# Performance work log

Hardware: AMD Instinct MI355X
Metric: run time of the kernel (lower is better)

The kernel has to match this reference:

```python
import jax, jax.numpy as jnp
import numpy as np
import math

N = 12288
D = 64
SCALE0 = math.log(10.0)


def lorentz_linear(x, W, b, scale):
    # x: [N, D] -> nn.Linear then Lorentz re-normalization onto the hyperboloid
    h = x @ W.T + b
    time = jax.nn.sigmoid(h[:, :1]) * jnp.exp(scale) + 1.1  # [N, 1]
    xn = h[:, 1:]  # spatial components [N, D-1]
    sq = jnp.clip(jnp.sum(xn * xn, axis=-1, keepdims=True), 1e-8, None)
    s = (time * time - 1.0) / sq
    return jnp.concatenate([time, xn * jnp.sqrt(s)], axis=-1)


def setup_inputs() -> dict:
    key = jax.random.key(0)
    ks = jax.random.split(key, 8)
    stdv = 1.0 / math.sqrt(D)
    x = jax.random.normal(ks[0], (N, D), dtype=jnp.float32)
    # sparse-ish binary adjacency stored dense (module calls adj.to_dense())
    adj = (jax.random.uniform(ks[1], (N, N)) < 0.002).astype(jnp.float32)
    W = jax.random.uniform(ks[2], (D, D), minval=-stdv, maxval=stdv, dtype=jnp.float32)
    Wq = jax.random.uniform(ks[3], (D, D), minval=-stdv, maxval=stdv, dtype=jnp.float32)
    Wk = jax.random.uniform(ks[4], (D, D), minval=-stdv, maxval=stdv, dtype=jnp.float32)
    z = jnp.zeros((D,), dtype=jnp.float32)
    sc = jnp.asarray(SCALE0, dtype=jnp.float32)
    return {
        'x': x, 'adj': adj,
        'W': W, 'b': z, 'scale': sc,
        'Wq': Wq, 'bq': z, 'scale_q': sc,
        'Wk': Wk, 'bk': z, 'scale_k': sc,
        'att_bias': jnp.asarray(20.0, dtype=jnp.float32),
        'att_scale': jnp.asarray(math.sqrt(D), dtype=jnp.float32),
    }


def reference(x, adj, W, b, scale, Wq, bq, scale_q, Wk, bk, scale_k, att_bias, att_scale):
    # LorentzLinear
    h = lorentz_linear(x, W, b, scale)  # [N, D]
    # LorentzAgg with attention
    q = lorentz_linear(h, Wq, bq, scale_q)
    k = lorentz_linear(h, Wk, bk, scale_k)
    # cinner: Lorentzian inner product matrix (negate time component of q)
    qm = jnp.concatenate([-q[:, :1], q[:, 1:]], axis=-1)
    att = 2.0 + 2.0 * (qm @ k.T)                 # [N, N]
    att = jax.nn.sigmoid(att / att_scale + att_bias)
    att = adj * att                               # mask by adjacency
    support = att @ h                             # [N, D]
    # Lorentz self-inner: inner(v,v) = -v0^2 + sum(v_rest^2); denorm = sqrt(|-inner|)
    inner = -support[:, :1] ** 2 + jnp.sum(support[:, 1:] ** 2, axis=-1, keepdims=True)
    denorm = jnp.sqrt(jnp.clip(jnp.abs(-inner), 1e-8, None))
    return support / denorm
```

## Files before the change

### kernel.cpp

```cpp
#include <hip/hip_runtime.h>
#include <math.h>

#define N 12288
#define D 64
#define CAP 96

__device__ __forceinline__ float wave_sum(float v) {
    #pragma unroll
    for (int m = 32; m >= 1; m >>= 1) v += __shfl_xor(v, m, 64);
    return v;
}

__global__ void lorentz_linear_kernel(const float* __restrict__ in,
                                      const float* __restrict__ W,
                                      const float* __restrict__ b,
                                      const float* __restrict__ scale,
                                      float* __restrict__ out,
                                      int negFirst) {
    __shared__ float Wlds[D * (D + 1)];
    int tid = threadIdx.x;
    for (int idx = tid; idx < D * D; idx += 256) {
        int d = idx >> 6, kk = idx & 63;
        Wlds[d * (D + 1) + kk] = W[idx];
    }
    __syncthreads();

    int lane = tid & 63;
    int row  = blockIdx.x * 4 + (tid >> 6);

    float xv  = in[row * D + lane];
    float acc = b[lane];
    const float* wr = &Wlds[lane * (D + 1)];
    #pragma unroll
    for (int kk = 0; kk < D; ++kk) {
        float xk = __shfl(xv, kk, 64);
        acc = fmaf(xk, wr[kk], acc);
    }

    float h0   = __shfl(acc, 0, 64);
    float es   = __expf(scale[0]);
    float time = es / (1.0f + __expf(-h0)) + 1.1f;
    float sq   = wave_sum((lane == 0) ? 0.0f : acc * acc);
    sq = fmaxf(sq, 1e-8f);
    float s = (time * time - 1.0f) / sq;
    float r = sqrtf(s);
    float o = (lane == 0) ? (negFirst ? -time : time) : acc * r;
    out[row * D + lane] = o;
}

__global__ void adj_scan_kernel(const float4* __restrict__ adj4,
                                int* __restrict__ cnt,
                                int* __restrict__ cols) {
    const int total = (N / 4) * N;
    int stride = gridDim.x * blockDim.x;
    for (int t = blockIdx.x * blockDim.x + threadIdx.x; t < total; t += stride) {
        float4 v = adj4[t];
        if (v.x == 0.0f && v.y == 0.0f && v.z == 0.0f && v.w == 0.0f) continue;
        int i = t / (N / 4);
        int jbase = (t - i * (N / 4)) * 4;
        float vals[4] = {v.x, v.y, v.z, v.w};
        #pragma unroll
        for (int c = 0; c < 4; ++c) {
            if (vals[c] != 0.0f) {
                int pos = atomicAdd(&cnt[i], 1);
                if (pos < CAP) cols[i * CAP + pos] = jbase + c;
            }
        }
    }
}

__global__ void gather_kernel(const float* __restrict__ qm,
                              const float* __restrict__ kmat,
                              const float* __restrict__ h,
                              const int* __restrict__ cnt,
                              const int* __restrict__ cols,
                              const float* __restrict__ att_bias_p,
                              const float* __restrict__ att_scale_p,
                              float* __restrict__ out) {
    int lane = threadIdx.x & 63;
    int row  = blockIdx.x * 4 + (threadIdx.x >> 6);

    float qv = qm[row * D + lane];
    int m = cnt[row]; if (m > CAP) m = CAP;
    float bias      = att_bias_p[0];
    float inv_scale = 1.0f / att_scale_p[0];

    float acc = 0.0f;
    for (int n = 0; n < m; ++n) {
        int j = cols[row * CAP + n];
        float dot = wave_sum(qv * kmat[j * D + lane]);
        float a   = fmaf(2.0f + 2.0f * dot, inv_scale, bias);
        float att = 1.0f / (1.0f + __expf(-a));
        acc = fmaf(att, h[j * D + lane], acc);
    }

    float contrib = (lane == 0) ? -acc * acc : acc * acc;
    float inner   = wave_sum(contrib);
    float denorm  = sqrtf(fmaxf(fabsf(inner), 1e-8f));
    out[row * D + lane] = acc / denorm;
}

extern "C" void kernel_launch(void* const* d_in, const int* in_sizes, int n_in,
                              void* d_out, int out_size, void* d_ws, size_t ws_size,
                              hipStream_t stream) {
    const float* x         = (const float*)d_in[0];
    const float* adj       = (const float*)d_in[1];
    const float* W         = (const float*)d_in[2];
    const float* b         = (const float*)d_in[3];
    const float* scale     = (const float*)d_in[4];
    const float* Wq        = (const float*)d_in[5];
    const float* bq        = (const float*)d_in[6];
    const float* scale_q   = (const float*)d_in[7];
    const float* Wk        = (const float*)d_in[8];
    const float* bk        = (const float*)d_in[9];
    const float* scale_k   = (const float*)d_in[10];
    const float* att_bias  = (const float*)d_in[11];
    const float* att_scale = (const float*)d_in[12];
    float* out = (float*)d_out;

    float* h    = (float*)d_ws;
    float* qm   = h  + (size_t)N * D;
    float* kmat = qm + (size_t)N * D;
    int*   cnt  = (int*)(kmat + (size_t)N * D);
    int*   cols = cnt + N;

    hipMemsetAsync(cnt, 0, N * sizeof(int), stream);

    lorentz_linear_kernel<<<N / 4, 256, 0, stream>>>(x, W, b, scale, h, 0);
    lorentz_linear_kernel<<<N / 4, 256, 0, stream>>>(h, Wq, bq, scale_q, qm, 1);
    lorentz_linear_kernel<<<N / 4, 256, 0, stream>>>(h, Wk, bk, scale_k, kmat, 0);

    adj_scan_kernel<<<2048, 256, 0, stream>>>((const float4*)adj, cnt, cols);

    gather_kernel<<<N / 4, 256, 0, stream>>>(qm, kmat, h, cnt, cols,
                                             att_bias, att_scale, out);
}
```

Before: 891.5 us.

## Fuse adjacency scan into gather kernel and merge Q/K projections

Each block now scans one adjacency row directly, collecting the nonzero columns in shared memory with LDS atomics. It then splits the neighbor loop across four waves and reduces their partial sums through LDS. This removes the global cnt/cols buffers, the memset, the global atomics and one kernel launch. The Q and K Lorentz projections are also fused into one kernel that reads h once. Using a uint4 bitwise test for zero treats -0.0 as nonzero, which is harmless for a 0/1 adjacency matrix.

```diff
diff --git a/kernel.cpp b/kernel.cpp
--- a/kernel.cpp
+++ b/kernel.cpp
@@ -11,12 +11,16 @@
     return v;
 }
 
-__global__ void lorentz_linear_kernel(const float* __restrict__ in,
-                                      const float* __restrict__ W,
-                                      const float* __restrict__ b,
-                                      const float* __restrict__ scale,
-                                      float* __restrict__ out,
-                                      int negFirst) {
+__device__ __forceinline__ float sigmoidf(float a) {
+    return 1.0f / (1.0f + __expf(-a));
+}
+
+__global__ __launch_bounds__(256) void lorentz_linear_kernel(
+        const float* __restrict__ in,
+        const float* __restrict__ W,
+        const float* __restrict__ b,
+        const float* __restrict__ scale,
+        float* __restrict__ out) {
     __shared__ float Wlds[D * (D + 1)];
     int tid = threadIdx.x;
     for (int idx = tid; idx < D * D; idx += 256) {
@@ -38,66 +42,118 @@
     }
 
     float h0   = __shfl(acc, 0, 64);
-    float es   = __expf(scale[0]);
-    float time = es / (1.0f + __expf(-h0)) + 1.1f;
-    float sq   = wave_sum((lane == 0) ? 0.0f : acc * acc);
-    sq = fmaxf(sq, 1e-8f);
-    float s = (time * time - 1.0f) / sq;
-    float r = sqrtf(s);
-    float o = (lane == 0) ? (negFirst ? -time : time) : acc * r;
-    out[row * D + lane] = o;
+    float time = __expf(scale[0]) * sigmoidf(h0) + 1.1f;
+    float sq   = fmaxf(wave_sum((lane == 0) ? 0.0f : acc * acc), 1e-8f);
+    float r    = sqrtf((time * time - 1.0f) / sq);
+    out[row * D + lane] = (lane == 0) ? time : acc * r;
 }
 
-__global__ void adj_scan_kernel(const float4* __restrict__ adj4,
-                                int* __restrict__ cnt,
-                                int* __restrict__ cols) {
-    const int total = (N / 4) * N;
-    int stride = gridDim.x * blockDim.x;
-    for (int t = blockIdx.x * blockDim.x + threadIdx.x; t < total; t += stride) {
-        float4 v = adj4[t];
-        if (v.x == 0.0f && v.y == 0.0f && v.z == 0.0f && v.w == 0.0f) continue;
-        int i = t / (N / 4);
-        int jbase = (t - i * (N / 4)) * 4;
-        float vals[4] = {v.x, v.y, v.z, v.w};
-        #pragma unroll
-        for (int c = 0; c < 4; ++c) {
-            if (vals[c] != 0.0f) {
-                int pos = atomicAdd(&cnt[i], 1);
-                if (pos < CAP) cols[i * CAP + pos] = jbase + c;
+__global__ __launch_bounds__(256) void lorentz_qk_kernel(
+        const float* __restrict__ h,
+        const float* __restrict__ Wq, const float* __restrict__ bq, const float* __restrict__ scale_q,
+        const float* __restrict__ Wk, const float* __restrict__ bk, const float* __restrict__ scale_k,
+        float* __restrict__ qm, float* __restrict__ kmat) {
+    __shared__ float Wqlds[D * (D + 1)];
+    __shared__ float Wklds[D * (D + 1)];
+    int tid = threadIdx.x;
+    for (int idx = tid; idx < D * D; idx += 256) {
+        int d = idx >> 6, kk = idx & 63;
+        Wqlds[d * (D + 1) + kk] = Wq[idx];
+        Wklds[d * (D + 1) + kk] = Wk[idx];
+    }
+    __syncthreads();
+
+    int lane = tid & 63;
+    int row  = blockIdx.x * 4 + (tid >> 6);
+
+    float hv   = h[row * D + lane];
+    float accq = bq[lane];
+    float acck = bk[lane];
+    const float* wq = &Wqlds[lane * (D + 1)];
+    const float* wk = &Wklds[lane * (D + 1)];
+    #pragma unroll
+    for (int kk = 0; kk < D; ++kk) {
+        float xk = __shfl(hv, kk, 64);
+        accq = fmaf(xk, wq[kk], accq);
+        acck = fmaf(xk, wk[kk], acck);
+    }
+
+    {
+        float h0   = __shfl(accq, 0, 64);
+        float time = __expf(scale_q[0]) * sigmoidf(h0) + 1.1f;
+        float sq   = fmaxf(wave_sum((lane == 0) ? 0.0f : accq * accq), 1e-8f);
+        float r    = sqrtf((time * time - 1.0f) / sq);
+        qm[row * D + lane] = (lane == 0) ? -time : accq * r;
+    }
+    {
+        float h0   = __shfl(acck, 0, 64);
+        float time = __expf(scale_k[0]) * sigmoidf(h0) + 1.1f;
+        float sq   = fmaxf(wave_sum((lane == 0) ? 0.0f : acck * acck), 1e-8f);
+        float r    = sqrtf((time * time - 1.0f) / sq);
+        kmat[row * D + lane] = (lane == 0) ? time : acck * r;
+    }
+}
+
+__global__ __launch_bounds__(256) void adj_gather_kernel(
+        const uint4* __restrict__ adj4,
+        const float* __restrict__ qm,
+        const float* __restrict__ kmat,
+        const float* __restrict__ h,
+        const float* __restrict__ att_bias_p,
+        const float* __restrict__ att_scale_p,
+        float* __restrict__ out) {
+    __shared__ int scols[CAP];
+    __shared__ int scnt;
+    __shared__ float sacc[4][D];
+
+    int tid  = threadIdx.x;
+    int row  = blockIdx.x;
+    if (tid == 0) scnt = 0;
+    __syncthreads();
+
+    const uint4* rowp = adj4 + (size_t)row * (N / 4);
+    #pragma unroll
+    for (int it = 0; it < (N / 4) / 256; ++it) {
+        int t = it * 256 + tid;
+        uint4 v = rowp[t];
+        if ((v.x | v.y | v.z | v.w) != 0u) {
+            unsigned e[4] = {v.x, v.y, v.z, v.w};
+            #pragma unroll
+            for (int c = 0; c < 4; ++c) {
+                if (e[c] != 0u) {
+                    int pos = atomicAdd(&scnt, 1);
+                    if (pos < CAP) scols[pos] = t * 4 + c;
+                }
             }
         }
     }
-}
+    __syncthreads();
 
-__global__ void gather_kernel(const float* __restrict__ qm,
-                              const float* __restrict__ kmat,
-                              const float* __restrict__ h,
-                              const int* __restrict__ cnt,
-                              const int* __restrict__ cols,
-                              const float* __restrict__ att_bias_p,
-                              const float* __restrict__ att_scale_p,
-                              float* __restrict__ out) {
-    int lane = threadIdx.x & 63;
-    int row  = blockIdx.x * 4 + (threadIdx.x >> 6);
+    int m = scnt; if (m > CAP) m = CAP;
+    int lane = tid & 63;
+    int w    = tid >> 6;
 
-    float qv = qm[row * D + lane];
-    int m = cnt[row]; if (m > CAP) m = CAP;
+    float qv        = qm[row * D + lane];
     float bias      = att_bias_p[0];
     float inv_scale = 1.0f / att_scale_p[0];
 
     float acc = 0.0f;
-    for (int n = 0; n < m; ++n) {
-        int j = cols[row * CAP + n];
+    for (int n = w; n < m; n += 4) {
+        int j = scols[n];
         float dot = wave_sum(qv * kmat[j * D + lane]);
-        float a   = fmaf(2.0f + 2.0f * dot, inv_scale, bias);
-        float att = 1.0f / (1.0f + __expf(-a));
+        float att = sigmoidf(fmaf(2.0f + 2.0f * dot, inv_scale, bias));
         acc = fmaf(att, h[j * D + lane], acc);
     }
+    sacc[w][lane] = acc;
+    __syncthreads();
 
-    float contrib = (lane == 0) ? -acc * acc : acc * acc;
-    float inner   = wave_sum(contrib);
-    float denorm  = sqrtf(fmaxf(fabsf(inner), 1e-8f));
-    out[row * D + lane] = acc / denorm;
+    if (w == 0) {
+        float total = sacc[0][lane] + sacc[1][lane] + sacc[2][lane] + sacc[3][lane];
+        float contrib = (lane == 0) ? -total * total : total * total;
+        float inner   = wave_sum(contrib);
+        float denorm  = sqrtf(fmaxf(fabsf(inner), 1e-8f));
+        out[row * D + lane] = total / denorm;
+    }
 }
 
 extern "C" void kernel_launch(void* const* d_in, const int* in_sizes, int n_in,
@@ -121,17 +177,10 @@
     float* h    = (float*)d_ws;
     float* qm   = h  + (size_t)N * D;
     float* kmat = qm + (size_t)N * D;
-    int*   cnt  = (int*)(kmat + (size_t)N * D);
-    int*   cols = cnt + N;
 
-    hipMemsetAsync(cnt, 0, N * sizeof(int), stream);
-
-    lorentz_linear_kernel<<<N / 4, 256, 0, stream>>>(x, W, b, scale, h, 0);
-    lorentz_linear_kernel<<<N / 4, 256, 0, stream>>>(h, Wq, bq, scale_q, qm, 1);
-    lorentz_linear_kernel<<<N / 4, 256, 0, stream>>>(h, Wk, bk, scale_k, kmat, 0);
-
-    adj_scan_kernel<<<2048, 256, 0, stream>>>((const float4*)adj, cnt, cols);
-
-    gather_kernel<<<N / 4, 256, 0, stream>>>(qm, kmat, h, cnt, cols,
+    lorentz_linear_kernel<<<N / 4, 256, 0, stream>>>(x, W, b, scale, h);
+    lorentz_qk_kernel<<<N / 4, 256, 0, stream>>>(h, Wq, bq, scale_q,
+                                                 Wk, bk, scale_k, qm, kmat);
+    adj_gather_kernel<<<N, 256, 0, stream>>>((const uint4*)adj, qm, kmat, h,
                                              att_bias, att_scale, out);
 }
```

Measured after the change: 824.2 us. -7.6%, faster.

## Fuse Lorentz linears and per-row adjacency scan into one kernel

Applied to the files above, without the earlier changes.

Merges the three Lorentz linear kernels and the adjacency scan into a single phase-one kernel. Each wavefront computes h, q and k for its row and then scans that row of adj with nontemporal loads, collecting column indices through LDS atomics before writing them out. This removes the memset, three kernel launches, the global atomics and the intermediate round trip of h between kernels. The cost is that the adjacency streaming, which dominates runtime, now runs inside a kernel with high LDS use, which may lower occupancy.

```diff
diff --git a/kernel.cpp b/kernel.cpp
--- a/kernel.cpp
+++ b/kernel.cpp
@@ -1,87 +1,127 @@
 #include <hip/hip_runtime.h>
 #include <math.h>
 
-#define N 12288
-#define D 64
+#define N   12288
+#define D   64
 #define CAP 96
+
+typedef unsigned int uint4n __attribute__((ext_vector_type(4)));
 
 __device__ __forceinline__ float wave_sum(float v) {
     #pragma unroll
     for (int m = 32; m >= 1; m >>= 1) v += __shfl_xor(v, m, 64);
     return v;
 }
+__device__ __forceinline__ float sigmoidf(float a) { return 1.0f / (1.0f + __expf(-a)); }
 
-__global__ void lorentz_linear_kernel(const float* __restrict__ in,
-                                      const float* __restrict__ W,
-                                      const float* __restrict__ b,
-                                      const float* __restrict__ scale,
-                                      float* __restrict__ out,
-                                      int negFirst) {
-    __shared__ float Wlds[D * (D + 1)];
-    int tid = threadIdx.x;
+__global__ __launch_bounds__(256) void phase1_kernel(
+        const float* __restrict__ x,
+        const uint4n* __restrict__ adj4,
+        const float* __restrict__ W,  const float* __restrict__ b,  const float* __restrict__ scale,
+        const float* __restrict__ Wq, const float* __restrict__ bq, const float* __restrict__ scale_q,
+        const float* __restrict__ Wk, const float* __restrict__ bk, const float* __restrict__ scale_k,
+        float* __restrict__ h, float* __restrict__ qm, float* __restrict__ kmat,
+        int* __restrict__ cnt, int* __restrict__ cols) {
+    __shared__ float Wl [D * (D + 1)];
+    __shared__ float Wql[D * (D + 1)];
+    __shared__ float Wkl[D * (D + 1)];
+    __shared__ unsigned short scols[4][CAP];
+    __shared__ int scnt[4];
+
+    const int tid  = threadIdx.x;
+    const int lane = tid & 63;
+    const int w    = tid >> 6;
+    const int row  = blockIdx.x * 4 + w;
+
     for (int idx = tid; idx < D * D; idx += 256) {
         int d = idx >> 6, kk = idx & 63;
-        Wlds[d * (D + 1) + kk] = W[idx];
+        Wl [d * (D + 1) + kk] = W [idx];
+        Wql[d * (D + 1) + kk] = Wq[idx];
+        Wkl[d * (D + 1) + kk] = Wk[idx];
     }
+    if (lane == 0) scnt[w] = 0;
     __syncthreads();
 
-    int lane = tid & 63;
-    int row  = blockIdx.x * 4 + (tid >> 6);
-
-    float xv  = in[row * D + lane];
-    float acc = b[lane];
-    const float* wr = &Wlds[lane * (D + 1)];
-    #pragma unroll
-    for (int kk = 0; kk < D; ++kk) {
-        float xk = __shfl(xv, kk, 64);
-        acc = fmaf(xk, wr[kk], acc);
+    float hvv;
+    {
+        float xv  = x[row * D + lane];
+        float acc = b[lane];
+        const float* wr = &Wl[lane * (D + 1)];
+        #pragma unroll
+        for (int kk = 0; kk < D; ++kk)
+            acc = fmaf(__shfl(xv, kk, 64), wr[kk], acc);
+        float h0   = __shfl(acc, 0, 64);
+        float time = __expf(scale[0]) * sigmoidf(h0) + 1.1f;
+        float sq   = fmaxf(wave_sum((lane == 0) ? 0.0f : acc * acc), 1e-8f);
+        float r    = sqrtf((time * time - 1.0f) / sq);
+        hvv = (lane == 0) ? time : acc * r;
+        h[row * D + lane] = hvv;
     }
 
-    float h0   = __shfl(acc, 0, 64);
-    float es   = __expf(scale[0]);
-    float time = es / (1.0f + __expf(-h0)) + 1.1f;
-    float sq   = wave_sum((lane == 0) ? 0.0f : acc * acc);
-    sq = fmaxf(sq, 1e-8f);
-    float s = (time * time - 1.0f) / sq;
-    float r = sqrtf(s);
-    float o = (lane == 0) ? (negFirst ? -time : time) : acc * r;
-    out[row * D + lane] = o;
-}
+    {
+        float accq = bq[lane], acck = bk[lane];
+        const float* wq = &Wql[lane * (D + 1)];
+        const float* wk = &Wkl[lane * (D + 1)];
+        #pragma unroll
+        for (int kk = 0; kk < D; ++kk) {
+            float xk = __shfl(hvv, kk, 64);
+            accq = fmaf(xk, wq[kk], accq);
+            acck = fmaf(xk, wk[kk], acck);
+        }
+        {
+            float h0   = __shfl(accq, 0, 64);
+            float time = __expf(scale_q[0]) * sigmoidf(h0) + 1.1f;
+            float sq   = fmaxf(wave_sum((lane == 0) ? 0.0f : accq * accq), 1e-8f);
+            float r    = sqrtf((time * time - 1.0f) / sq);
+            qm[row * D + lane] = (lane == 0) ? -time : accq * r;
+        }
+        {
+            float h0   = __shfl(acck, 0, 64);
+            float time = __expf(scale_k[0]) * sigmoidf(h0) + 1.1f;
+            float sq   = fmaxf(wave_sum((lane == 0) ? 0.0f : acck * acck), 1e-8f);
+            float r    = sqrtf((time * time - 1.0f) / sq);
+            kmat[row * D + lane] = (lane == 0) ? time : acck * r;
+        }
+    }
 
-__global__ void adj_scan_kernel(const float4* __restrict__ adj4,
-                                int* __restrict__ cnt,
-                                int* __restrict__ cols) {
-    const int total = (N / 4) * N;
-    int stride = gridDim.x * blockDim.x;
-    for (int t = blockIdx.x * blockDim.x + threadIdx.x; t < total; t += stride) {
-        float4 v = adj4[t];
-        if (v.x == 0.0f && v.y == 0.0f && v.z == 0.0f && v.w == 0.0f) continue;
-        int i = t / (N / 4);
-        int jbase = (t - i * (N / 4)) * 4;
-        float vals[4] = {v.x, v.y, v.z, v.w};
-        #pragma unroll
-        for (int c = 0; c < 4; ++c) {
-            if (vals[c] != 0.0f) {
-                int pos = atomicAdd(&cnt[i], 1);
-                if (pos < CAP) cols[i * CAP + pos] = jbase + c;
+    {
+        const uint4n* rp = adj4 + (size_t)row * (N / 4);
+        #pragma unroll 4
+        for (int it = 0; it < (N / 4) / 64; ++it) {
+            int t = it * 64 + lane;
+            uint4n v = __builtin_nontemporal_load(&rp[t]);
+            if ((v.x | v.y | v.z | v.w) != 0u) {
+                unsigned e[4] = {v.x, v.y, v.z, v.w};
+                #pragma unroll
+                for (int c = 0; c < 4; ++c) {
+                    if (e[c] != 0u) {
+                        int pos = atomicAdd(&scnt[w], 1);
+                        if (pos < CAP) scols[w][pos] = (unsigned short)(t * 4 + c);
+                    }
+                }
             }
         }
+        int m = scnt[w]; if (m > CAP) m = CAP;
+        if (lane == 0) cnt[row] = m;
+        for (int n = lane; n < m; n += 64)
+            cols[row * CAP + n] = scols[w][n];
     }
 }
 
-__global__ void gather_kernel(const float* __restrict__ qm,
-                              const float* __restrict__ kmat,
-                              const float* __restrict__ h,
-                              const int* __restrict__ cnt,
-                              const int* __restrict__ cols,
-                              const float* __restrict__ att_bias_p,
-                              const float* __restrict__ att_scale_p,
-                              float* __restrict__ out) {
+__global__ __launch_bounds__(256) void gather_kernel(
+        const float* __restrict__ qm,
+        const float* __restrict__ kmat,
+        const float* __restrict__ h,
+        const int* __restrict__ cnt,
+        const int* __restrict__ cols,
+        const float* __restrict__ att_bias_p,
+        const float* __restrict__ att_scale_p,
+        float* __restrict__ out) {
     int lane = threadIdx.x & 63;
     int row  = blockIdx.x * 4 + (threadIdx.x >> 6);
 
     float qv = qm[row * D + lane];
-    int m = cnt[row]; if (m > CAP) m = CAP;
+    int m = cnt[row];
     float bias      = att_bias_p[0];
     float inv_scale = 1.0f / att_scale_p[0];
 
@@ -89,8 +129,7 @@
     for (int n = 0; n < m; ++n) {
         int j = cols[row * CAP + n];
         float dot = wave_sum(qv * kmat[j * D + lane]);
-        float a   = fmaf(2.0f + 2.0f * dot, inv_scale, bias);
-        float att = 1.0f / (1.0f + __expf(-a));
+        float att = sigmoidf(fmaf(2.0f + 2.0f * dot, inv_scale, bias));
         acc = fmaf(att, h[j * D + lane], acc);
     }
 
@@ -103,35 +142,30 @@
 extern "C" void kernel_launch(void* const* d_in, const int* in_sizes, int n_in,
                               void* d_out, int out_size, void* d_ws, size_t ws_size,
                               hipStream_t stream) {
-    const float* x         = (const float*)d_in[0];
-    const float* adj       = (const float*)d_in[1];
-    const float* W         = (const float*)d_in[2];
-    const float* b         = (const float*)d_in[3];
-    const float* scale     = (const float*)d_in[4];
-    const float* Wq        = (const float*)d_in[5];
-    const float* bq        = (const float*)d_in[6];
-    const float* scale_q   = (const float*)d_in[7];
-    const float* Wk        = (const float*)d_in[8];
-    const float* bk        = (const float*)d_in[9];
-    const float* scale_k   = (const float*)d_in[10];
-    const float* att_bias  = (const float*)d_in[11];
-    const float* att_scale = (const float*)d_in[12];
+    const float*  x         = (const float*)d_in[0];
+    const uint4n* adj       = (const uint4n*)d_in[1];
+    const float*  W         = (const float*)d_in[2];
+    const float*  b         = (const float*)d_in[3];
+    const float*  scale     = (const float*)d_in[4];
+    const float*  Wq        = (const float*)d_in[5];
+    const float*  bq        = (const float*)d_in[6];
+    const float*  scale_q   = (const float*)d_in[7];
+    const float*  Wk        = (const float*)d_in[8];
+    const float*  bk        = (const float*)d_in[9];
+    const float*  scale_k   = (const float*)d_in[10];
+    const float*  att_bias  = (const float*)d_in[11];
+    const float*  att_scale = (const float*)d_in[12];
     float* out = (float*)d_out;
 
     float* h    = (float*)d_ws;
-    float* qm   = h  + (size_t)N * D;
-    float* kmat = qm + (size_t)N * D;
+    float* qm   = h    + (size_t)N * D;
+    float* kmat = qm   + (size_t)N * D;
     int*   cnt  = (int*)(kmat + (size_t)N * D);
     int*   cols = cnt + N;
 
-    hipMemsetAsync(cnt, 0, N * sizeof(int), stream);
-
-    lorentz_linear_kernel<<<N / 4, 256, 0, stream>>>(x, W, b, scale, h, 0);
-    lorentz_linear_kernel<<<N / 4, 256, 0, stream>>>(h, Wq, bq, scale_q, qm, 1);
-    lorentz_linear_kernel<<<N / 4, 256, 0, stream>>>(h, Wk, bk, scale_k, kmat, 0);
-
-    adj_scan_kernel<<<2048, 256, 0, stream>>>((const float4*)adj, cnt, cols);
-
+    phase1_kernel<<<N / 4, 256, 0, stream>>>(x, adj, W, b, scale,
+                                             Wq, bq, scale_q, Wk, bk, scale_k,
+                                             h, qm, kmat, cnt, cols);
     gather_kernel<<<N / 4, 256, 0, stream>>>(qm, kmat, h, cnt, cols,
                                              att_bias, att_scale, out);
 }
```

New measurement: 851.5 us. 4.5% less time.
